# Kernel optimization log

Hardware: AMD Instinct MI355X
Metric: run time of the kernel (lower is better)

The kernel has to match this reference:

```python
import jax, jax.numpy as jnp
import numpy as np

MAX_WAVELENGTH = 10000.0
NUM_HEADS = 15
NUM_KV_HEADS = 5
HEAD_DIM = 64


def apply_rope(x, positions):
    """RoPE: x [B, L, H, D], positions [B, L] (int)."""
    d_half = x.shape[-1] // 2
    x = x.astype(jnp.float32)
    freq_exponents = (2.0 / x.shape[-1]) * jnp.arange(d_half, dtype=jnp.float32)
    timescale = MAX_WAVELENGTH ** freq_exponents  # [d_half]
    radians = positions[..., None].astype(jnp.float32) / timescale  # [B, L, d_half]
    radians = radians[..., None, :]  # [B, L, 1, d_half]
    sin, cos = jnp.sin(radians), jnp.cos(radians)
    x1, x2 = x[..., :d_half], x[..., d_half:]
    return jnp.concatenate([x1 * cos - x2 * sin, x2 * cos + x1 * sin], axis=-1)


def setup_inputs() -> dict:
    key = jax.random.key(0)
    k1, k2, k3, k4 = jax.random.split(key, 4)
    B, L = 2, 2048
    query_states = jax.random.normal(k1, (B, L, NUM_HEADS, HEAD_DIM), dtype=jnp.float32)
    key_states = jax.random.normal(k2, (B, L, NUM_KV_HEADS, HEAD_DIM), dtype=jnp.float32)
    value_states = jax.random.normal(k3, (B, L, NUM_KV_HEADS, HEAD_DIM), dtype=jnp.float32)
    positions = jnp.sort(jax.random.randint(k4, (B, L), 0, L, dtype=jnp.int32), axis=-1)
    # Causal (prefix-LM) boolean mask [B, L, L]
    attention_mask = jnp.broadcast_to(jnp.tril(jnp.ones((L, L), dtype=bool)), (B, L, L))
    return {
        "query_states": query_states,
        "key_states": key_states,
        "value_states": value_states,
        "positions": positions,
        "attention_mask": attention_mask,
    }


def reference(query_states, key_states, value_states, positions, attention_mask):
    B, L = query_states.shape[0], query_states.shape[1]
    groups = NUM_HEADS // NUM_KV_HEADS  # 3

    # RoPE on Q and K (eager, per original module)
    q = apply_rope(query_states, positions)  # [B, L, 15, 64] fp32
    k = apply_rope(key_states, positions)    # [B, L, 5, 64]  fp32

    # GQA expansion: [B, L, Kv, D] -> [B, L, Kv*groups, D]
    k = jnp.repeat(k, groups, axis=2)
    v = jnp.repeat(value_states, groups, axis=2).astype(jnp.float32)

    # Scores in fp32: [B, H, Lq, Lk]
    scores = jnp.einsum("bqhd,bkhd->bhqk", q, k) * (HEAD_DIM ** -0.5)
    big_neg = jnp.finfo(jnp.float32).min
    scores = jnp.where(attention_mask[:, None, :, :], scores, big_neg)
    probs = jax.nn.softmax(scores, axis=-1)

    out = jnp.einsum("bhqk,bkhd->bqhd", probs, v)  # [B, L, H, D]
    return out.reshape(B, L, NUM_HEADS * HEAD_DIM)  # [B, L, 960]
```

## Files before the change

### kernel.cpp

```cpp
#include <hip/hip_runtime.h>
#include <math.h>

#define NB 2
#define NL 2048
#define NHQ 15
#define NKV 5
#define HD 64
#define NT 32
#define GRP 3
#define PST 72

typedef __attribute__((ext_vector_type(8))) short short8;
typedef __attribute__((ext_vector_type(4))) float floatx4;

#define ROPE_C 0.28782313662425575f
#define QSCALE 0.18033688011116016f

__device__ __forceinline__ ushort f2bf(float x) {
    unsigned u = __builtin_bit_cast(unsigned, x);
    u = (u + 0x7FFFu + ((u >> 16) & 1u)) >> 16;
    return (ushort)u;
}
__device__ __forceinline__ unsigned pk2(float a, float b) {
    unsigned ua = __builtin_bit_cast(unsigned, a) + 0x8000u;
    unsigned ub = __builtin_bit_cast(unsigned, b) + 0x8000u;
    return __builtin_amdgcn_perm(ub, ua, 0x07060302u);
}

union U8  { short8 v; ushort u[8]; };
union F8  { float4 f4[2]; float f[8]; };

__global__ __launch_bounds__(256)
void prep_kv(const float* __restrict__ K, const float* __restrict__ V,
             const int* __restrict__ pos, ushort* __restrict__ Kr,
             ushort* __restrict__ Vr) {
    __shared__ float Vs[64][65];
    const int bid = blockIdx.x, t = threadIdx.x;
    if (bid < NB * NKV * NT) {
        int b = bid / (NKV * NT), rem = bid % (NKV * NT);
        int h = rem / NT, k0 = (rem % NT) * 64;
        int j = t >> 2, c0 = t & 3;
        int row = k0 + j;
        const float* src = K + ((size_t)((b * NL + row) * NKV + h)) * HD;
        int db = c0 * 8;
        F8 x1, x2;
        x1.f4[0] = *(const float4*)&src[db];
        x1.f4[1] = *(const float4*)&src[db + 4];
        x2.f4[0] = *(const float4*)&src[db + 32];
        x2.f4[1] = *(const float4*)&src[db + 36];
        float ps = (float)pos[b * NL + row];
        U8 lo, hi;
#pragma unroll
        for (int i = 0; i < 8; ++i) {
            float inv = __expf((float)(db + i) * -ROPE_C);
            float sn, cs; __sincosf(ps * inv, &sn, &cs);
            lo.u[i] = f2bf(x1.f[i] * cs - x2.f[i] * sn);
            hi.u[i] = f2bf(x2.f[i] * cs + x1.f[i] * sn);
        }
        ushort* dst = Kr + (size_t)bid * 4096;
        *(short8*)&dst[(((j >> 4)) * 64 + c0 * 16 + (j & 15)) * 8]     = lo.v;
        *(short8*)&dst[((4 + (j >> 4)) * 64 + c0 * 16 + (j & 15)) * 8] = hi.v;
    } else {
        int vb = bid - NB * NKV * NT;
        int b = vb / (NKV * NT), rem = vb % (NKV * NT);
        int h = rem / NT, k0 = (rem % NT) * 64;
#pragma unroll
        for (int it = 0; it < 4; ++it) {
            int e = t + it * 256;
            int j = e >> 4, d4 = (e & 15) * 4;
            *(float4*)&Vs[j][d4] =
                *(const float4*)&V[((size_t)((b * NL + k0 + j) * NKV + h)) * HD + d4];
        }
        __syncthreads();
        ushort* dst = Vr + (size_t)vb * 4096;
#pragma unroll
        for (int it = 0; it < 2; ++it) {
            int o = t + it * 256;
            int d = o >> 3, c = o & 7, j0 = c * 8;
            U8 r;
#pragma unroll
            for (int k = 0; k < 8; ++k) r.u[k] = f2bf(Vs[j0 + k][d]);
            *(short8*)&dst[(((c >> 2) * 4 + (d >> 4)) * 64 + (c & 3) * 16 + (d & 15)) * 8] = r.v;
        }
    }
}

__device__ __forceinline__ void tile_step(
    int kb, bool diag, int r0, int l16, int quad,
    const short8 (&kc)[8], const short8 (&vc)[8],
    const short8 (&Qa)[2][2], floatx4 (&O)[2][4], float (&lsum)[2],
    ushort (&PbW)[2][16 * PST])
{
    floatx4 S[2][4];
#pragma unroll
    for (int rf = 0; rf < 2; ++rf)
#pragma unroll
        for (int c = 0; c < 4; ++c) S[rf][c] = (floatx4){0.f, 0.f, 0.f, 0.f};
#pragma unroll
    for (int s = 0; s < 2; ++s)
#pragma unroll
        for (int c = 0; c < 4; ++c) {
            short8 kfv = kc[s * 4 + c];
            S[0][c] = __builtin_amdgcn_mfma_f32_16x16x32_bf16(kfv, Qa[0][s], S[0][c], 0, 0, 0);
            S[1][c] = __builtin_amdgcn_mfma_f32_16x16x32_bf16(kfv, Qa[1][s], S[1][c], 0, 0, 0);
        }

    if (diag) {
#pragma unroll
        for (int rf = 0; rf < 2; ++rf) {
            int qrow = r0 + rf * 16 + l16;
            float acc = 0.f;
#pragma unroll
            for (int c = 0; c < 4; ++c) {
                float pv[4];
#pragma unroll
                for (int r = 0; r < 4; ++r) {
                    int key = kb * 64 + c * 16 + quad * 4 + r;
                    float sv = S[rf][c][r];
                    if (key > qrow) sv = -1e30f;
                    pv[r] = exp2f(sv);
                    acc += pv[r];
                }
                *(uint2*)&PbW[rf][l16 * PST + c * 16 + quad * 4] =
                    make_uint2(pk2(pv[0], pv[1]), pk2(pv[2], pv[3]));
            }
            lsum[rf] += acc;
        }
    } else {
#pragma unroll
        for (int rf = 0; rf < 2; ++rf) {
            float acc = 0.f;
#pragma unroll
            for (int c = 0; c < 4; ++c) {
                float pv[4];
#pragma unroll
                for (int r = 0; r < 4; ++r) {
                    pv[r] = exp2f(S[rf][c][r]);
                    acc += pv[r];
                }
                *(uint2*)&PbW[rf][l16 * PST + c * 16 + quad * 4] =
                    make_uint2(pk2(pv[0], pv[1]), pk2(pv[2], pv[3]));
            }
            lsum[rf] += acc;
        }
    }

#pragma unroll
    for (int s = 0; s < 2; ++s) {
        short8 pf0 = *(const short8*)&PbW[0][l16 * PST + s * 32 + quad * 8];
        short8 pf1 = *(const short8*)&PbW[1][l16 * PST + s * 32 + quad * 8];
#pragma unroll
        for (int d = 0; d < 4; ++d) {
            short8 vfv = vc[s * 4 + d];
            O[0][d] = __builtin_amdgcn_mfma_f32_16x16x32_bf16(vfv, pf0, O[0][d], 0, 0, 0);
            O[1][d] = __builtin_amdgcn_mfma_f32_16x16x32_bf16(vfv, pf1, O[1][d], 0, 0, 0);
        }
    }
}

#define LOADT(KD, VD, tile)                                                   \
    {                                                                         \
        const ushort* _kt = Kt0 + (size_t)(tile) * 4096;                      \
        const ushort* _vt = Vt0 + (size_t)(tile) * 4096;                      \
        _Pragma("unroll")                                                     \
        for (int _i = 0; _i < 8; ++_i) {                                      \
            KD[_i] = *(const short8*)&_kt[((size_t)_i * 64 + lane) * 8];      \
            VD[_i] = *(const short8*)&_vt[((size_t)_i * 64 + lane) * 8];      \
        }                                                                     \
    }

__global__ __launch_bounds__(256, 2)
void attn_flash(const float* __restrict__ Q, const ushort* __restrict__ Kr,
                const ushort* __restrict__ Vr, const int* __restrict__ pos,
                float* __restrict__ out) {
    __shared__ __align__(16) ushort Pb[4][2][16 * PST];

    const int t = threadIdx.x;
    const int w = t >> 6, lane = t & 63;
    const int l16 = lane & 15, quad = lane >> 4;

    const int bid  = blockIdx.x;
    const int work = (bid & 7) * 60 + (bid >> 3);
    const int bh = work >> 4;
    const int k  = work & 15;
    const int b = bh / NHQ, h = bh % NHQ;
    const int kvh = h / GRP;
    const int qi = (w == 0) ? k : (w == 1) ? (31 - k) : (w == 2) ? (32 + k) : (63 - k);
    const int ntw = (qi >> 1) + 1;
    const int r0  = qi * 32;

    const ushort* Kt0 = Kr + (size_t)((b * NKV + kvh) * NT) * 4096;
    const ushort* Vt0 = Vr + (size_t)((b * NKV + kvh) * NT) * 4096;

    short8 Qa[2][2];
#pragma unroll
    for (int rf = 0; rf < 2; ++rf) {
        int row = r0 + rf * 16 + l16;
        const float* src = Q + ((size_t)((b * NL + row) * NHQ + h)) * HD;
        int db = quad * 8;
        F8 x1, x2;
        x1.f4[0] = *(const float4*)&src[db];
        x1.f4[1] = *(const float4*)&src[db + 4];
        x2.f4[0] = *(const float4*)&src[db + 32];
        x2.f4[1] = *(const float4*)&src[db + 36];
        float ps = (float)pos[b * NL + row];
        union { short8 v; unsigned u[4]; } lo, hi;
#pragma unroll
        for (int i = 0; i < 8; i += 2) {
            float inv0 = __expf((float)(db + i) * -ROPE_C);
            float inv1 = __expf((float)(db + i + 1) * -ROPE_C);
            float sn0, cs0, sn1, cs1;
            __sincosf(ps * inv0, &sn0, &cs0);
            __sincosf(ps * inv1, &sn1, &cs1);
            float lo0 = (x1.f[i] * cs0 - x2.f[i] * sn0) * QSCALE;
            float lo1 = (x1.f[i + 1] * cs1 - x2.f[i + 1] * sn1) * QSCALE;
            float hi0 = (x2.f[i] * cs0 + x1.f[i] * sn0) * QSCALE;
            float hi1 = (x2.f[i + 1] * cs1 + x1.f[i + 1] * sn1) * QSCALE;
            lo.u[i >> 1] = pk2(lo0, lo1);
            hi.u[i >> 1] = pk2(hi0, hi1);
        }
        Qa[rf][0] = lo.v;
        Qa[rf][1] = hi.v;
    }

    floatx4 O[2][4];
    float lsum[2] = {0.f, 0.f};
#pragma unroll
    for (int rf = 0; rf < 2; ++rf)
#pragma unroll
        for (int d = 0; d < 4; ++d) O[rf][d] = (floatx4){0.f, 0.f, 0.f, 0.f};

    short8 kA[8], vA[8], kB[8], vB[8];
    LOADT(kA, vA, 0);
    int kb = 0;
    for (;;) {
        if (kb + 1 < ntw) LOADT(kB, vB, kb + 1);
        __builtin_amdgcn_sched_barrier(0);
        tile_step(kb, kb == ntw - 1, r0, l16, quad, kA, vA, Qa, O, lsum, Pb[w]);
        if (++kb >= ntw) break;

        if (kb + 1 < ntw) LOADT(kA, vA, kb + 1);
        __builtin_amdgcn_sched_barrier(0);
        tile_step(kb, kb == ntw - 1, r0, l16, quad, kB, vB, Qa, O, lsum, Pb[w]);
        if (++kb >= ntw) break;
    }

#pragma unroll
    for (int rf = 0; rf < 2; ++rf) {
        float ls = lsum[rf];
        ls += __shfl_xor(ls, 16, 64);
        ls += __shfl_xor(ls, 32, 64);
        float rinv = 1.0f / ls;
        int qrow = r0 + rf * 16 + l16;
        float* op = out + (size_t)(b * NL + qrow) * (NHQ * HD) + h * HD;
#pragma unroll
        for (int d = 0; d < 4; ++d) {
            float4 o = make_float4(O[rf][d][0] * rinv, O[rf][d][1] * rinv,
                                   O[rf][d][2] * rinv, O[rf][d][3] * rinv);
            *(float4*)&op[d * 16 + quad * 4] = o;
        }
    }
}

extern "C" void kernel_launch(void* const* d_in, const int* in_sizes, int n_in,
                              void* d_out, int out_size, void* d_ws, size_t ws_size,
                              hipStream_t stream) {
    const float* Q   = (const float*)d_in[0];
    const float* K   = (const float*)d_in[1];
    const float* V   = (const float*)d_in[2];
    const int*   pos = (const int*)d_in[3];
    ushort* Kr = (ushort*)d_ws;
    ushort* Vr = Kr + (size_t)NB * NKV * NT * 4096;
    float*  out = (float*)d_out;

    prep_kv<<<2 * NB * NKV * NT, 256, 0, stream>>>(K, V, pos, Kr, Vr);
    attn_flash<<<NB * NHQ * 16, 256, 0, stream>>>(Q, Kr, Vr, pos, out);
}
```

Baseline: 138.6 us.

## Split long causal query rows across waves with split-K and LDS combine

```diff
diff --git a/kernel.cpp b/kernel.cpp
--- a/kernel.cpp
+++ b/kernel.cpp
@@ -9,6 +9,9 @@
 #define NT 32
 #define GRP 3
 #define PST 72
+#define NWB 40
+#define CST 68
+#define CSLOT (32 * CST + 32)
 
 typedef __attribute__((ext_vector_type(8))) short short8;
 typedef __attribute__((ext_vector_type(4))) float floatx4;
@@ -89,7 +92,7 @@
     int kb, bool diag, int r0, int l16, int quad,
     const short8 (&kc)[8], const short8 (&vc)[8],
     const short8 (&Qa)[2][2], floatx4 (&O)[2][4], float (&lsum)[2],
-    ushort (&PbW)[2][16 * PST])
+    ushort* PbW)
 {
     floatx4 S[2][4];
 #pragma unroll
@@ -121,7 +124,7 @@
                     pv[r] = exp2f(sv);
                     acc += pv[r];
                 }
-                *(uint2*)&PbW[rf][l16 * PST + c * 16 + quad * 4] =
+                *(uint2*)&PbW[rf * 16 * PST + l16 * PST + c * 16 + quad * 4] =
                     make_uint2(pk2(pv[0], pv[1]), pk2(pv[2], pv[3]));
             }
             lsum[rf] += acc;
@@ -138,7 +141,7 @@
                     pv[r] = exp2f(S[rf][c][r]);
                     acc += pv[r];
                 }
-                *(uint2*)&PbW[rf][l16 * PST + c * 16 + quad * 4] =
+                *(uint2*)&PbW[rf * 16 * PST + l16 * PST + c * 16 + quad * 4] =
                     make_uint2(pk2(pv[0], pv[1]), pk2(pv[2], pv[3]));
             }
             lsum[rf] += acc;
@@ -147,8 +150,8 @@
 
 #pragma unroll
     for (int s = 0; s < 2; ++s) {
-        short8 pf0 = *(const short8*)&PbW[0][l16 * PST + s * 32 + quad * 8];
-        short8 pf1 = *(const short8*)&PbW[1][l16 * PST + s * 32 + quad * 8];
+        short8 pf0 = *(const short8*)&PbW[0 * 16 * PST + l16 * PST + s * 32 + quad * 8];
+        short8 pf1 = *(const short8*)&PbW[1 * 16 * PST + l16 * PST + s * 32 + quad * 8];
 #pragma unroll
         for (int d = 0; d < 4; ++d) {
             short8 vfv = vc[s * 4 + d];
@@ -169,28 +172,42 @@
         }                                                                     \
     }
 
-__global__ __launch_bounds__(256, 2)
+__global__ __launch_bounds__(256, 4)
 void attn_flash(const float* __restrict__ Q, const ushort* __restrict__ Kr,
                 const ushort* __restrict__ Vr, const int* __restrict__ pos,
                 float* __restrict__ out) {
-    __shared__ __align__(16) ushort Pb[4][2][16 * PST];
+    __shared__ __align__(16) unsigned char smem[3 * CSLOT * sizeof(float)];
 
     const int t = threadIdx.x;
     const int w = t >> 6, lane = t & 63;
     const int l16 = lane & 15, quad = lane >> 4;
 
     const int bid  = blockIdx.x;
-    const int work = (bid & 7) * 60 + (bid >> 3);
-    const int bh = work >> 4;
-    const int k  = work & 15;
+    const int work = (bid & 7) * 150 + (bid >> 3);
+    const int bh   = work / NWB;
+    const int beta = work % NWB;
     const int b = bh / NHQ, h = bh % NHQ;
     const int kvh = h / GRP;
-    const int qi = (w == 0) ? k : (w == 1) ? (31 - k) : (w == 2) ? (32 + k) : (63 - k);
-    const int ntw = (qi >> 1) + 1;
-    const int r0  = qi * 32;
+
+    int qi, leaderw, nch;
+    if (beta < 16)      { qi = 48 + beta; leaderw = 0; nch = 4; }
+    else if (beta < 32) {
+        if (w < 3)      { qi = 32 + (beta - 16); leaderw = 0; nch = 3; }
+        else            { qi = beta - 16;        leaderw = 3; nch = 1; }
+    } else {
+        int c = beta - 32;
+        if (w < 2)      { qi = 16 + 2 * c; leaderw = 0; nch = 2; }
+        else            { qi = 17 + 2 * c; leaderw = 2; nch = 2; }
+    }
+    const int ntw   = (qi >> 1) + 1;
+    const int chunk = w - leaderw;
+    const int kb0   = (ntw * chunk) / nch;
+    const int kb1   = (ntw * (chunk + 1)) / nch;
+    const int r0    = qi * 32;
 
     const ushort* Kt0 = Kr + (size_t)((b * NKV + kvh) * NT) * 4096;
     const ushort* Vt0 = Vr + (size_t)((b * NKV + kvh) * NT) * 4096;
+    ushort* PbW = (ushort*)smem + w * 2 * 16 * PST;
 
     short8 Qa[2][2];
 #pragma unroll
@@ -230,34 +247,61 @@
 #pragma unroll
         for (int d = 0; d < 4; ++d) O[rf][d] = (floatx4){0.f, 0.f, 0.f, 0.f};
 
-    short8 kA[8], vA[8], kB[8], vB[8];
-    LOADT(kA, vA, 0);
-    int kb = 0;
-    for (;;) {
-        if (kb + 1 < ntw) LOADT(kB, vB, kb + 1);
-        __builtin_amdgcn_sched_barrier(0);
-        tile_step(kb, kb == ntw - 1, r0, l16, quad, kA, vA, Qa, O, lsum, Pb[w]);
-        if (++kb >= ntw) break;
-
-        if (kb + 1 < ntw) LOADT(kA, vA, kb + 1);
-        __builtin_amdgcn_sched_barrier(0);
-        tile_step(kb, kb == ntw - 1, r0, l16, quad, kB, vB, Qa, O, lsum, Pb[w]);
-        if (++kb >= ntw) break;
-    }
-
+    for (int kb = kb0; kb < kb1; ++kb) {
+        short8 kc[8], vc[8];
+        LOADT(kc, vc, kb);
+        tile_step(kb, kb == ntw - 1, r0, l16, quad, kc, vc, Qa, O, lsum, PbW);
+    }
+
+    float ls[2];
 #pragma unroll
     for (int rf = 0; rf < 2; ++rf) {
-        float ls = lsum[rf];
-        ls += __shfl_xor(ls, 16, 64);
-        ls += __shfl_xor(ls, 32, 64);
-        float rinv = 1.0f / ls;
-        int qrow = r0 + rf * 16 + l16;
-        float* op = out + (size_t)(b * NL + qrow) * (NHQ * HD) + h * HD;
-#pragma unroll
-        for (int d = 0; d < 4; ++d) {
-            float4 o = make_float4(O[rf][d][0] * rinv, O[rf][d][1] * rinv,
-                                   O[rf][d][2] * rinv, O[rf][d][3] * rinv);
-            *(float4*)&op[d * 16 + quad * 4] = o;
+        float v = lsum[rf];
+        v += __shfl_xor(v, 16, 64);
+        v += __shfl_xor(v, 32, 64);
+        ls[rf] = v;
+    }
+
+    __syncthreads();
+    float* Cmb = (float*)smem;
+    if (chunk > 0) {
+        float* slot = Cmb + (size_t)(w - 1) * CSLOT;
+#pragma unroll
+        for (int rf = 0; rf < 2; ++rf) {
+#pragma unroll
+            for (int d = 0; d < 4; ++d) {
+                *(float4*)&slot[(rf * 16 + l16) * CST + d * 16 + quad * 4] =
+                    make_float4(O[rf][d][0], O[rf][d][1], O[rf][d][2], O[rf][d][3]);
+            }
+            if (quad == 0) slot[32 * CST + rf * 16 + l16] = ls[rf];
+        }
+    }
+    __syncthreads();
+    if (chunk == 0) {
+        for (int m = 1; m < nch; ++m) {
+            const float* slot = Cmb + (size_t)(w + m - 1) * CSLOT;
+#pragma unroll
+            for (int rf = 0; rf < 2; ++rf) {
+#pragma unroll
+                for (int d = 0; d < 4; ++d) {
+                    float4 x = *(const float4*)&slot[(rf * 16 + l16) * CST + d * 16 + quad * 4];
+                    O[rf][d][0] += x.x; O[rf][d][1] += x.y;
+                    O[rf][d][2] += x.z; O[rf][d][3] += x.w;
+                }
+                ls[rf] += slot[32 * CST + rf * 16 + l16];
+            }
+        }
+#pragma unroll
+        for (int rf = 0; rf < 2; ++rf) {
+            float rinv = 1.0f / ls[rf];
+            int qrow = r0 + rf * 16 + l16;
+            float* op = out + (size_t)(b * NL + qrow) * (NHQ * HD) + h * HD;
+#pragma unroll
+            for (int d = 0; d < 4; ++d) {
+                float4 o = make_float4(O[rf][d][0] * rinv, O[rf][d][1] * rinv,
+                                       O[rf][d][2] * rinv, O[rf][d][3] * rinv);
+                *(float4*)&op[d * 16 + quad * 4] = o;
+            }
         }
     }
 }
@@ -274,5 +318,5 @@
     float*  out = (float*)d_out;
 
     prep_kv<<<2 * NB * NKV * NT, 256, 0, stream>>>(K, V, pos, Kr, Vr);
-    attn_flash<<<NB * NHQ * 16, 256, 0, stream>>>(Q, Kr, Vr, pos, out);
-}
+    attn_flash<<<NB * NHQ * NWB, 256, 0, stream>>>(Q, Kr, Vr, pos, out);
+}
```

Result: slower. 171.6 us (+23.8%).
